# Kernel optimization log

Hardware: AMD Instinct MI355X
Metric: run time of the kernel (lower is better)

The kernel has to match this reference:

```python
import jax, jax.numpy as jnp
import numpy as np

B, S, WIDTH, M = 2, 240, 128, 20
PAD = 16


def setup_inputs() -> dict:
    key = jax.random.key(0)
    ks = jax.random.split(key, 10)
    scale = 1.0 / (WIDTH * WIDTH)
    inp = {
        "x": jax.random.normal(ks[0], (B, S, S, 3), jnp.float32),
        "fc0_w": jax.random.normal(ks[1], (5, WIDTH), jnp.float32) * 0.1,
        "fc0_b": jnp.zeros((WIDTH,), jnp.float32),
        # 5 spectral layers, complex weights stored as [..., 2] = (real, imag)
        "spec_w1": jax.random.uniform(ks[2], (5, WIDTH, WIDTH, M, M, 2), jnp.float32) * scale,
        "spec_w2": jax.random.uniform(ks[3], (5, WIDTH, WIDTH, M, M, 2), jnp.float32) * scale,
        # 5 residual 1x1 convs
        "w_w": jax.random.normal(ks[4], (5, WIDTH, WIDTH), jnp.float32) / np.sqrt(WIDTH),
        "w_b": jnp.zeros((5, WIDTH), jnp.float32),
        "fc1_w": jax.random.normal(ks[5], (WIDTH, WIDTH), jnp.float32) / np.sqrt(WIDTH),
        "fc1_b": jnp.zeros((WIDTH,), jnp.float32),
        # 4 heads (u, v, p, T): width->64->1
        "head1_w": jax.random.normal(ks[6], (4, WIDTH, 64), jnp.float32) / np.sqrt(WIDTH),
        "head1_b": jnp.zeros((4, 64), jnp.float32),
        "head2_w": jax.random.normal(ks[7], (4, 64, 1), jnp.float32) / 8.0,
        "head2_b": jnp.zeros((4, 1), jnp.float32),
    }
    return inp


def _spectral_conv(h, w1, w2):
    # h: (B, C, H, W) real; w1, w2: (C_in, C_out, M, M) complex64
    Hh, Ww = h.shape[-2], h.shape[-1]
    ft = jnp.fft.rfft2(h)  # (B, C, H, W//2+1)
    o1 = jnp.einsum('bixy,ioxy->boxy', ft[:, :, :M, :M], w1)
    o2 = jnp.einsum('bixy,ioxy->boxy', ft[:, :, -M:, :M], w2)
    out_ft = jnp.zeros((h.shape[0], w1.shape[1], Hh, Ww // 2 + 1), jnp.complex64)
    out_ft = out_ft.at[:, :, :M, :M].set(o1).at[:, :, -M:, :M].set(o2)
    return jnp.fft.irfft2(out_ft, s=(Hh, Ww))


def reference(x, fc0_w, fc0_b, spec_w1, spec_w2, w_w, w_b, fc1_w, fc1_b,
              head1_w, head1_b, head2_w, head2_b):
    Bn, sx, sy = x.shape[0], x.shape[1], x.shape[2]
    gx = jnp.broadcast_to(jnp.linspace(0.0, 1.0, sx, dtype=x.dtype)[None, :, None, None], (Bn, sx, sy, 1))
    gy = jnp.broadcast_to(jnp.linspace(0.0, 1.0, sy, dtype=x.dtype)[None, None, :, None], (Bn, sx, sy, 1))
    x1 = jnp.concatenate([x, gx, gy], axis=-1)          # (B, S, S, 5)
    h = x1 @ fc0_w + fc0_b                              # lift -> (B, S, S, width)
    h = jnp.transpose(h, (0, 3, 1, 2))                  # (B, width, S, S)
    h = jnp.pad(h, ((0, 0), (0, 0), (0, PAD), (0, PAD)))
    c1 = spec_w1[..., 0] + 1j * spec_w1[..., 1]
    c2 = spec_w2[..., 0] + 1j * spec_w2[..., 1]
    for i in range(5):
        s = _spectral_conv(h, c1[i], c2[i])
        lin = jnp.einsum('bchw,oc->bohw', h, w_w[i]) + w_b[i][None, :, None, None]
        h = s + lin
        if i < 4:
            h = jax.nn.gelu(h, approximate=False)
    h = h[..., :-PAD, :-PAD]
    h = jnp.transpose(h, (0, 2, 3, 1))                  # (B, S, S, width)
    h = jax.nn.gelu(h @ fc1_w + fc1_b, approximate=False)
    h1 = jax.nn.gelu(jnp.einsum('bhwc,kcd->kbhwd', h, head1_w)
                     + head1_b[:, None, None, None, :], approximate=False)
    out = jnp.einsum('kbhwd,kdo->kbhwo', h1, head2_w) + head2_b[:, None, None, None, :]
    return (out[0], out[1], out[2], out[3])  # u, v, p, T each (B, S, S, 1)
```

## Files before the change

kernel.cpp:

```cpp
#include <hip/hip_runtime.h>
#include <math.h>


#define SZ_H   (2ull*256*256*128)
#define O_HA   0ull
#define O_HB   (O_HA + SZ_H)
#define O_G    (O_HB + SZ_H)
#define SZ_G   (2ull*256*20*128*2)
#define O_FTT  (O_G + SZ_G)
#define SZ_FT  (2ull*40*20*128*2)
#define O_OFT  (O_FTT + SZ_FT)
#define O_EY   (O_OFT + SZ_FT)
#define SZ_EY  (256ull*20*2)
#define O_EX   (O_EY + SZ_EY)
#define SZ_EX  (256ull*40*2)
#define O_EXI  (O_EX + SZ_EX)
#define O_WWT  (O_EXI + SZ_EX)
#define SZ_WWT 81920ull
#define O_PART (O_WWT + SZ_WWT)
#define SZ_PART (8ull*204800*2)
#define FC1_B_NEED (O_G + 6356992ull)

static __device__ __forceinline__ float gelu_f(float v) {
    return 0.5f * v * (1.0f + erff(v * 0.70710678118654752f));
}

__global__ void k_prep(const float* __restrict__ w_w, float* __restrict__ ws) {
    int i = blockIdx.x * 256 + threadIdx.x;
    const float STEP = 6.2831853071795864769f / 256.0f;
    if (i < 5120) {
        int ky = i % 20, y = i / 20;
        int t = (ky * y) & 255;
        float th = t * STEP;
        ws[O_EY + 2*(size_t)i]     = cosf(th);
        ws[O_EY + 2*(size_t)i + 1] = -sinf(th);
    } else if (i < 15360) {
        int m = i - 5120; int j = m % 40, x = m / 40;
        int kx = (j < 20) ? j : (216 + j);
        int t = (kx * x) & 255;
        float th = t * STEP;
        ws[O_EX + 2*(size_t)m]     = cosf(th);
        ws[O_EX + 2*(size_t)m + 1] = -sinf(th);
    } else if (i < 25600) {
        int m = i - 15360; int j = m % 40, x = m / 40;
        int kx = (j < 20) ? j : (216 + j);
        int t = (kx * x) & 255;
        float th = t * STEP;
        ws[O_EXI + 2*(size_t)m]     = cosf(th);
        ws[O_EXI + 2*(size_t)m + 1] = sinf(th);
    } else {
        int m = i - 25600;
        if (m < 81920) {
            int l = m >> 14, r = m & 16383;
            int ic = r >> 7, oc = r & 127;
            ws[O_WWT + m] = w_w[(size_t)l*16384 + oc*128 + ic];
        }
    }
}

__global__ __launch_bounds__(256) void k_fc0(const float* __restrict__ xin,
        const float* __restrict__ w, const float* __restrict__ bv,
        float4* __restrict__ H4) {
    size_t e = (size_t)blockIdx.x * 256 + threadIdx.x;
    int c4 = (int)(e & 31) * 4;
    int y = (int)((e >> 5) & 255);
    int x = (int)((e >> 13) & 255);
    int b = (int)(e >> 21);
    float4 h = make_float4(0.f, 0.f, 0.f, 0.f);
    if (x < 240 && y < 240) {
        const float* xp = xin + (((size_t)(b*240 + x))*240 + y)*3;
        float x0 = xp[0], x1 = xp[1], x2 = xp[2];
        float gx = x*(1.0f/239.0f), gy = y*(1.0f/239.0f);
        float4 w0 = *(const float4*)&w[c4];
        float4 w1 = *(const float4*)&w[128 + c4];
        float4 w2 = *(const float4*)&w[256 + c4];
        float4 w3 = *(const float4*)&w[384 + c4];
        float4 w4 = *(const float4*)&w[512 + c4];
        float4 bb = *(const float4*)&bv[c4];
        h.x = bb.x + x0*w0.x + x1*w1.x + x2*w2.x + gx*w3.x + gy*w4.x;
        h.y = bb.y + x0*w0.y + x1*w1.y + x2*w2.y + gx*w3.y + gy*w4.y;
        h.z = bb.z + x0*w0.z + x1*w1.z + x2*w2.z + gx*w3.z + gy*w4.z;
        h.w = bb.w + x0*w0.w + x1*w1.w + x2*w2.w + gx*w3.w + gy*w4.w;
    }
    H4[e] = h;
}

__global__ __launch_bounds__(256) void k_ydft(const float* __restrict__ H,
        const float* __restrict__ Ey, float2* __restrict__ G) {
    int b = blockIdx.x >> 8, x = blockIdx.x & 255;
    int c = threadIdx.x & 127;
    int yq = __builtin_amdgcn_readfirstlane((int)(threadIdx.x >> 7));
    const float* Hrow = H + ((size_t)(b*256 + x)) * 256 * 128;
    float ar[20], ai[20];
    #pragma unroll
    for (int k = 0; k < 20; k++) { ar[k] = 0.f; ai[k] = 0.f; }
    for (int i = 0; i < 128; i++) {
        int y = yq*128 + i;
        float v = Hrow[(size_t)y*128 + c];
        const float* e = Ey + (size_t)y*40;
        #pragma unroll
        for (int k = 0; k < 20; k++) {
            ar[k] = fmaf(v, e[2*k],   ar[k]);
            ai[k] = fmaf(v, e[2*k+1], ai[k]);
        }
    }
    __shared__ float red[20][128][2];
    if (yq == 1) {
        #pragma unroll
        for (int k = 0; k < 20; k++) { red[k][c][0] = ar[k]; red[k][c][1] = ai[k]; }
    }
    __syncthreads();
    if (yq == 0) {
        float2* Gp = G + ((size_t)(b*256 + x))*20*128;
        #pragma unroll
        for (int k = 0; k < 20; k++)
            Gp[k*128 + c] = make_float2(ar[k] + red[k][c][0], ai[k] + red[k][c][1]);
    }
}

__global__ __launch_bounds__(512) void k_xdft(const float2* __restrict__ G,
        const float* __restrict__ Ex, float2* __restrict__ ftT) {
    int t = blockIdx.x;
    int ch = t & 1, jq = (t >> 1) & 1, ky = (t >> 2) % 20, b = t / 80;
    int cl = threadIdx.x & 63;
    int xq = __builtin_amdgcn_readfirstlane((int)(threadIdx.x >> 6));
    int c = ch*64 + cl;
    int j0 = jq * 20;
    float ar[20], ai[20];
    #pragma unroll
    for (int k = 0; k < 20; k++) { ar[k] = 0.f; ai[k] = 0.f; }
    for (int i = 0; i < 32; i++) {
        int x = xq*32 + i;
        float2 g = G[(((size_t)(b*256 + x))*20 + ky)*128 + c];
        const float* e = Ex + (size_t)x*80 + j0*2;
        #pragma unroll
        for (int k = 0; k < 20; k++) {
            float er = e[2*k], ei = e[2*k+1];
            ar[k] = fmaf(g.x, er, fmaf(-g.y, ei, ar[k]));
            ai[k] = fmaf(g.x, ei, fmaf( g.y, er, ai[k]));
        }
    }
    __shared__ float red[4][20][64][2];
    if (xq >= 4) {
        int s = xq - 4;
        #pragma unroll
        for (int k = 0; k < 20; k++) { red[s][k][cl][0] = ar[k]; red[s][k][cl][1] = ai[k]; }
    }
    __syncthreads();
    if (xq < 4) {
        #pragma unroll
        for (int k = 0; k < 20; k++) { ar[k] += red[xq][k][cl][0]; ai[k] += red[xq][k][cl][1]; }
    }
    __syncthreads();
    if (xq == 2 || xq == 3) {
        int s = xq - 2;
        #pragma unroll
        for (int k = 0; k < 20; k++) { red[s][k][cl][0] = ar[k]; red[s][k][cl][1] = ai[k]; }
    }
    __syncthreads();
    if (xq < 2) {
        #pragma unroll
        for (int k = 0; k < 20; k++) { ar[k] += red[xq][k][cl][0]; ai[k] += red[xq][k][cl][1]; }
    }
    __syncthreads();
    if (xq == 1) {
        #pragma unroll
        for (int k = 0; k < 20; k++) { red[0][k][cl][0] = ar[k]; red[0][k][cl][1] = ai[k]; }
    }
    __syncthreads();
    if (xq == 0) {
        #pragma unroll
        for (int k = 0; k < 20; k++) {
            float rr = ar[k] + red[0][k][cl][0];
            float ii = ai[k] + red[0][k][cl][1];
            ftT[((size_t)c*2 + b)*800 + (size_t)(j0 + k)*20 + ky] = make_float2(rr, ii);
        }
    }
}

__global__ __launch_bounds__(448) void k_modemix(const float2* __restrict__ w1,
        const float2* __restrict__ w2, const float2* __restrict__ ftT,
        float2* __restrict__ outp, int ic_per) {
    int bid = blockIdx.x & 255;
    int icq = blockIdx.x >> 8;
    int oc = bid >> 1;
    int mh = bid & 1;
    int tid = threadIdx.x;
    if (tid >= 400) return;
    int wsel = tid / 200;
    int m = mh*200 + (tid % 200);
    int jk = wsel*400 + m;
    const float2* wb = wsel ? w2 : w1;
    int ic0 = icq * ic_per;
    float ar0=0.f, ai0=0.f, ar1=0.f, ai1=0.f;
    #pragma unroll 4
    for (int i = 0; i < ic_per; i++) {
        int ic = ic0 + i;
        float2 wv = wb[((size_t)(ic*128 + oc))*400 + m];
        float2 f0 = ftT[(size_t)ic*1600 + jk];
        float2 f1 = ftT[(size_t)ic*1600 + 800 + jk];
        ar0 = fmaf(f0.x, wv.x, fmaf(-f0.y, wv.y, ar0));
        ai0 = fmaf(f0.x, wv.y, fmaf( f0.y, wv.x, ai0));
        ar1 = fmaf(f1.x, wv.x, fmaf(-f1.y, wv.y, ar1));
        ai1 = fmaf(f1.x, wv.y, fmaf( f1.y, wv.x, ai1));
    }
    float2* o = outp + (size_t)icq * 204800;
    o[(size_t)jk*128 + oc]         = make_float2(ar0, ai0);
    o[(size_t)(800 + jk)*128 + oc] = make_float2(ar1, ai1);
}

__global__ __launch_bounds__(512) void k_modered(const float2* __restrict__ part,
        float2* __restrict__ oft) {
    int i = blockIdx.x * 512 + threadIdx.x;
    if (i >= 204800) return;
    float2 s = part[i];
    #pragma unroll
    for (int q = 1; q < 8; q++) {
        float2 p = part[(size_t)q*204800 + i];
        s.x += p.x; s.y += p.y;
    }
    oft[i] = s;
}

__global__ __launch_bounds__(256) void k_xidft(const float2* __restrict__ oft,
        const float* __restrict__ Exi, float2* __restrict__ T) {
    int b = blockIdx.x >> 7, xq = blockIdx.x & 127;
    int oc = threadIdx.x & 127;
    int xs = __builtin_amdgcn_readfirstlane((int)(threadIdx.x >> 7));
    int x = xq*2 + xs;
    float ar[20], ai[20];
    #pragma unroll
    for (int k = 0; k < 20; k++) { ar[k] = 0.f; ai[k] = 0.f; }
    const float2* ob = oft + (size_t)b*800*128;
    for (int j = 0; j < 40; j++) {
        float er = Exi[(size_t)x*80 + 2*j], ei = Exi[(size_t)x*80 + 2*j + 1];
        #pragma unroll
        for (int k = 0; k < 20; k++) {
            float2 o = ob[(size_t)(j*20 + k)*128 + oc];
            ar[k] = fmaf(o.x, er, fmaf(-o.y, ei, ar[k]));
            ai[k] = fmaf(o.x, ei, fmaf( o.y, er, ai[k]));
        }
    }
    float2* Tp = T + ((size_t)(b*256 + x))*20*128;
    #pragma unroll
    for (int k = 0; k < 20; k++) Tp[k*128 + oc] = make_float2(ar[k], ai[k]);
}

__global__ __launch_bounds__(256) void k_spec_lin(const float* __restrict__ H,
        const float2* __restrict__ T, const float* __restrict__ wwT,
        const float* __restrict__ wb, float* __restrict__ Hout, int do_gelu) {
    int yg = blockIdx.x & 3;
    int x  = (blockIdx.x >> 2) & 255;
    int b  = blockIdx.x >> 10;
    int tid = threadIdx.x;
    int lane = tid & 63;
    int wv = __builtin_amdgcn_readfirstlane(tid >> 6);
    int oc0 = wv * 32;
    int y0 = yg * 64;
    __shared__ float hl[64][129];
    const float* Hbase = H + (((size_t)(b*256 + x))*256 + y0)*128;
    #pragma unroll
    for (int it = 0; it < 8; it++) {
        int i = tid + it*256;
        int pi = i >> 5, c4 = (i & 31)*4;
        float4 v = *(const float4*)&Hbase[(size_t)pi*128 + c4];
        hl[pi][c4] = v.x; hl[pi][c4+1] = v.y; hl[pi][c4+2] = v.z; hl[pi][c4+3] = v.w;
    }
    float csr[20], csi[20];
    {
        int y = y0 + lane;
        #pragma unroll
        for (int k = 0; k < 20; k++) {
            int t = (k * y) & 255;
            float th = t * (6.2831853071795864769f/256.0f);
            float f = (k == 0 ? 1.0f : 2.0f) * (1.0f/65536.0f);
            csr[k] = f * __cosf(th);
            csi[k] = f * __sinf(th);
        }
    }
    __syncthreads();
    float acc[32];
    #pragma unroll
    for (int o = 0; o < 32; o++) acc[o] = 0.f;
    for (int ic = 0; ic < 128; ic++) {
        float t = hl[lane][ic];
        const float* wr = &wwT[(size_t)ic*128 + oc0];
        #pragma unroll
        for (int o4 = 0; o4 < 8; o4++) {
            float4 w = *(const float4*)&wr[o4*4];
            acc[o4*4]   = fmaf(t, w.x, acc[o4*4]);
            acc[o4*4+1] = fmaf(t, w.y, acc[o4*4+1]);
            acc[o4*4+2] = fmaf(t, w.z, acc[o4*4+2]);
            acc[o4*4+3] = fmaf(t, w.w, acc[o4*4+3]);
        }
    }
    const float2* Tp = T + ((size_t)(b*256 + x))*20*128 + oc0;
    for (int k = 0; k < 20; k++) {
        const float2* tr = Tp + (size_t)k*128;
        float cr = csr[k], ci = csi[k];
        #pragma unroll
        for (int o = 0; o < 32; o++) {
            float2 tv = tr[o];
            acc[o] = fmaf(tv.x, cr, fmaf(-tv.y, ci, acc[o]));
        }
    }
    __syncthreads();
    const float* bp = &wb[oc0];
    #pragma unroll
    for (int o = 0; o < 32; o++) {
        float v = acc[o] + bp[o];
        if (do_gelu) v = gelu_f(v);
        hl[lane][oc0 + o] = v;
    }
    __syncthreads();
    float* Obase = Hout + (((size_t)(b*256 + x))*256 + y0)*128;
    #pragma unroll
    for (int it = 0; it < 32; it++) {
        int i = tid + it*256;
        int pi = i >> 7, c = i & 127;
        Obase[(size_t)pi*128 + c] = hl[pi][c];
    }
}

__global__ __launch_bounds__(128) void k_fc1(const float* __restrict__ H,
        const float* __restrict__ fc1_w, const float* __restrict__ fc1_b,
        float* __restrict__ outA, float* __restrict__ outB) {
    int tid = threadIdx.x;
    int lane = tid & 63;
    int wv = __builtin_amdgcn_readfirstlane(tid >> 6);
    int p0 = blockIdx.x * 64;
    __shared__ float hl[64][129];
    #pragma unroll
    for (int it = 0; it < 16; it++) {
        int i = tid + it*128;
        int pi = i >> 5, c4 = (i & 31)*4;
        int p = p0 + pi;
        int bb = p / 57600, r = p % 57600;
        int xx = r / 240, yy = r % 240;
        float4 v = *(const float4*)&H[(((size_t)(bb*256 + xx))*256 + yy)*128 + c4];
        hl[pi][c4] = v.x; hl[pi][c4+1] = v.y; hl[pi][c4+2] = v.z; hl[pi][c4+3] = v.w;
    }
    __syncthreads();
    int oc0 = wv*64;
    float acc[64];
    #pragma unroll
    for (int o = 0; o < 64; o++) acc[o] = 0.f;
    for (int ic = 0; ic < 128; ic++) {
        float t = hl[lane][ic];
        const float* wr = &fc1_w[(size_t)ic*128 + oc0];
        #pragma unroll
        for (int o4 = 0; o4 < 16; o4++) {
            float4 w = *(const float4*)&wr[o4*4];
            acc[o4*4]   = fmaf(t, w.x, acc[o4*4]);
            acc[o4*4+1] = fmaf(t, w.y, acc[o4*4+1]);
            acc[o4*4+2] = fmaf(t, w.z, acc[o4*4+2]);
            acc[o4*4+3] = fmaf(t, w.w, acc[o4*4+3]);
        }
    }
    __syncthreads();
    const float* bp = &fc1_b[oc0];
    #pragma unroll
    for (int o = 0; o < 64; o++) hl[lane][oc0 + o] = gelu_f(acc[o] + bp[o]);
    __syncthreads();
    float* outp = (p0 < 65536) ? (outA + (size_t)p0*128)
                               : (outB + ((size_t)(p0 - 65536))*128);
    #pragma unroll
    for (int it = 0; it < 64; it++) {
        int i = tid + it*128;
        int pi = i >> 7, c = i & 127;
        outp[(size_t)pi*128 + c] = hl[pi][c];
    }
}

__global__ __launch_bounds__(256) void k_heads(const float* __restrict__ inA,
        const float* __restrict__ inB, const float* __restrict__ h1w,
        const float* __restrict__ h1b, const float* __restrict__ h2w,
        const float* __restrict__ h2b, float* __restrict__ out) {
    int tid = threadIdx.x;
    int lane = tid & 63;
    int k = __builtin_amdgcn_readfirstlane(tid >> 6);
    int p0 = blockIdx.x * 64;
    __shared__ float tl[128][65];
    const float* inp = (p0 < 65536) ? (inA + (size_t)p0*128)
                                    : (inB + ((size_t)(p0 - 65536))*128);
    #pragma unroll
    for (int it = 0; it < 8; it++) {
        int i = tid + it*256;
        int pi = i >> 5, c4 = (i & 31)*4;
        float4 v = *(const float4*)&inp[(size_t)pi*128 + c4];
        tl[c4][pi] = v.x; tl[c4+1][pi] = v.y; tl[c4+2][pi] = v.z; tl[c4+3][pi] = v.w;
    }
    __syncthreads();
    float acc[64];
    #pragma unroll
    for (int d = 0; d < 64; d++) acc[d] = 0.f;
    const float* wk = h1w + (size_t)k*8192;
    for (int c = 0; c < 128; c++) {
        float t = tl[c][lane];
        const float* wr = &wk[c*64];
        #pragma unroll
        for (int d4 = 0; d4 < 16; d4++) {
            float4 w = *(const float4*)&wr[d4*4];
            acc[d4*4]   = fmaf(t, w.x, acc[d4*4]);
            acc[d4*4+1] = fmaf(t, w.y, acc[d4*4+1]);
            acc[d4*4+2] = fmaf(t, w.z, acc[d4*4+2]);
            acc[d4*4+3] = fmaf(t, w.w, acc[d4*4+3]);
        }
    }
    const float* b1 = &h1b[k*64];
    const float* w2 = &h2w[k*64];
    float res = 0.f;
    #pragma unroll
    for (int d = 0; d < 64; d++)
        res += gelu_f(acc[d] + b1[d]) * w2[d];
    out[(size_t)k*115200 + p0 + lane] = res + h2b[k];
}

__global__ __launch_bounds__(256) void k_head(const float* __restrict__ H,
        const float* __restrict__ fc1_w, const float* __restrict__ fc1_b,
        const float* __restrict__ h1w, const float* __restrict__ h1b,
        const float* __restrict__ h2w, const float* __restrict__ h2b,
        float* __restrict__ out) {
    int tid = threadIdx.x;
    int p0 = blockIdx.x * 64;
    __shared__ float hl[64][128];
    __shared__ float tl[128][65];
    #pragma unroll
    for (int it = 0; it < 8; it++) {
        int i = tid + it*256;
        int pi = i >> 5, c4 = (i & 31)*4;
        int p = p0 + pi;
        int b = p / 57600, r = p % 57600;
        int xx = r / 240, yy = r % 240;
        *(float4*)&hl[pi][c4] = *(const float4*)&H[(((size_t)(b*256 + xx))*256 + yy)*128 + c4];
    }
    __syncthreads();
    {
        int ocg = tid & 31, pxg = tid >> 5;
        int oc0 = ocg*4, px0 = pxg*8;
        float acc[4][8];
        #pragma unroll
        for (int q = 0; q < 4; q++)
            #pragma unroll
            for (int p = 0; p < 8; p++) acc[q][p] = 0.f;
        for (int icc = 0; icc < 32; icc++) {
            float4 hv[8];
            #pragma unroll
            for (int p = 0; p < 8; p++) hv[p] = *(float4*)&hl[px0 + p][icc*4];
            float4 wA = *(const float4*)&fc1_w[(size_t)(icc*4+0)*128 + oc0];
            float4 wB = *(const float4*)&fc1_w[(size_t)(icc*4+1)*128 + oc0];
            float4 wC = *(const float4*)&fc1_w[(size_t)(icc*4+2)*128 + oc0];
            float4 wD = *(const float4*)&fc1_w[(size_t)(icc*4+3)*128 + oc0];
            #pragma unroll
            for (int p = 0; p < 8; p++) {
                float4 h4 = hv[p];
                acc[0][p] = fmaf(h4.x, wA.x, fmaf(h4.y, wB.x, fmaf(h4.z, wC.x, fmaf(h4.w, wD.x, acc[0][p]))));
                acc[1][p] = fmaf(h4.x, wA.y, fmaf(h4.y, wB.y, fmaf(h4.z, wC.y, fmaf(h4.w, wD.y, acc[1][p]))));
                acc[2][p] = fmaf(h4.x, wA.z, fmaf(h4.y, wB.z, fmaf(h4.z, wC.z, fmaf(h4.w, wD.z, acc[2][p]))));
                acc[3][p] = fmaf(h4.x, wA.w, fmaf(h4.y, wB.w, fmaf(h4.z, wC.w, fmaf(h4.w, wD.w, acc[3][p]))));
            }
        }
        float4 bb = *(const float4*)&fc1_b[oc0];
        float bq[4] = {bb.x, bb.y, bb.z, bb.w};
        #pragma unroll
        for (int q = 0; q < 4; q++)
            #pragma unroll
            for (int p = 0; p < 8; p++)
                tl[oc0 + q][px0 + p] = gelu_f(acc[q][p] + bq[q]);
    }
    __syncthreads();
    {
        int k = tid >> 6, dg = tid & 15, pxg = (tid >> 4) & 3;
        int d0 = dg*4, px0 = pxg*16;
        float acc2[4][16];
        #pragma unroll
        for (int q = 0; q < 4; q++)
            #pragma unroll
            for (int i = 0; i < 16; i++) acc2[q][i] = 0.f;
        const float* wp = h1w + (size_t)k*8192 + d0;
        for (int c = 0; c < 128; c++) {
            float4 w = *(const float4*)&wp[(size_t)c*64];
            #pragma unroll
            for (int i = 0; i < 16; i++) {
                float v = tl[c][px0 + i];
                acc2[0][i] = fmaf(v, w.x, acc2[0][i]);
                acc2[1][i] = fmaf(v, w.y, acc2[1][i]);
                acc2[2][i] = fmaf(v, w.z, acc2[2][i]);
                acc2[3][i] = fmaf(v, w.w, acc2[3][i]);
            }
        }
        float4 b1 = *(const float4*)&h1b[k*64 + d0];
        float4 w2 = *(const float4*)&h2w[k*64 + d0];
        float ob = h2b[k];
        #pragma unroll
        for (int i = 0; i < 16; i++) {
            float u = gelu_f(acc2[0][i] + b1.x) * w2.x
                    + gelu_f(acc2[1][i] + b1.y) * w2.y
                    + gelu_f(acc2[2][i] + b1.z) * w2.z
                    + gelu_f(acc2[3][i] + b1.w) * w2.w;
            u += __shfl_down(u, 8);
            u += __shfl_down(u, 4);
            u += __shfl_down(u, 2);
            u += __shfl_down(u, 1);
            if (dg == 0) out[(size_t)k*115200 + p0 + px0 + i] = u + ob;
        }
    }
}

extern "C" void kernel_launch(void* const* d_in, const int* in_sizes, int n_in,
                              void* d_out, int out_size, void* d_ws, size_t ws_size,
                              hipStream_t stream) {
    const float* x       = (const float*)d_in[0];
    const float* fc0_w   = (const float*)d_in[1];
    const float* fc0_b   = (const float*)d_in[2];
    const float* spec_w1 = (const float*)d_in[3];
    const float* spec_w2 = (const float*)d_in[4];
    const float* w_w     = (const float*)d_in[5];
    const float* w_b     = (const float*)d_in[6];
    const float* fc1_w   = (const float*)d_in[7];
    const float* fc1_b   = (const float*)d_in[8];
    const float* head1_w = (const float*)d_in[9];
    const float* head1_b = (const float*)d_in[10];
    const float* head2_w = (const float*)d_in[11];
    const float* head2_b = (const float*)d_in[12];
    float* ws = (float*)d_ws;
    float* out = (float*)d_out;

    int split      = ws_size >= (size_t)(O_PART + SZ_PART) * 4 ? 1 : 0;
    int head_split = ws_size >= (size_t)FC1_B_NEED * 4 ? 1 : 0;

    k_prep<<<420, 256, 0, stream>>>(w_w, ws);
    k_fc0<<<16384, 256, 0, stream>>>(x, fc0_w, fc0_b, (float4*)(ws + O_HA));

    float* cur = ws + O_HA;
    float* nxt = ws + O_HB;
    float2* G    = (float2*)(ws + O_G);
    float2* ftT  = (float2*)(ws + O_FTT);
    float2* oft  = (float2*)(ws + O_OFT);
    float2* part = (float2*)(ws + O_PART);

    for (int l = 0; l < 5; l++) {
        k_ydft<<<512, 256, 0, stream>>>(cur, ws + O_EY, G);
        k_xdft<<<160, 512, 0, stream>>>(G, ws + O_EX, ftT);
        const float2* w1l = (const float2*)(spec_w1 + (size_t)l*13107200);
        const float2* w2l = (const float2*)(spec_w2 + (size_t)l*13107200);
        if (split) {
            k_modemix<<<2048, 448, 0, stream>>>(w1l, w2l, ftT, part, 16);
            k_modered<<<400, 512, 0, stream>>>(part, oft);
        } else {
            k_modemix<<<256, 448, 0, stream>>>(w1l, w2l, ftT, oft, 128);
        }
        k_xidft<<<256, 256, 0, stream>>>(oft, ws + O_EXI, G);
        k_spec_lin<<<2048, 256, 0, stream>>>(cur, G, ws + O_WWT + (size_t)l*16384,
                                             w_b + l*128, nxt, (l < 4) ? 1 : 0);
        float* t = cur; cur = nxt; nxt = t;
    }
    if (head_split) {
        float* fA = ws + O_HA;
        float* fB = ws + O_G;
        k_fc1<<<1800, 128, 0, stream>>>(cur, fc1_w, fc1_b, fA, fB);
        k_heads<<<1800, 256, 0, stream>>>(fA, fB, head1_w, head1_b,
                                          head2_w, head2_b, out);
    } else {
        k_head<<<1800, 256, 0, stream>>>(cur, fc1_w, fc1_b, head1_w, head1_b,
                                         head2_w, head2_b, out);
    }
}
```

Measured before the change: 1.960 ms.

## Fuse fc1 and heads into one tail kernel and repartition x-DFT blocks

Merges the separate fc1 and heads kernels into one 512-thread kernel. The fc1 output stays in shared memory (transposed) and feeds the four heads directly, so the intermediate activation no longer makes a global round trip. Also splits the x-direction DFT over four times as many smaller blocks, with fewer accumulators per thread and a shuffle plus single shared-memory reduction step instead of a multi-stage barrier tree. The fused kernel's many global weight loads per thread, and the higher per-block register and LDS use, may limit occupancy.

```diff
diff --git a/kernel.cpp b/kernel.cpp
--- a/kernel.cpp
+++ b/kernel.cpp
@@ -19,7 +19,6 @@
 #define SZ_WWT 81920ull
 #define O_PART (O_WWT + SZ_WWT)
 #define SZ_PART (8ull*204800*2)
-#define FC1_B_NEED (O_G + 6356992ull)
 
 static __device__ __forceinline__ float gelu_f(float v) {
     return 0.5f * v * (1.0f + erff(v * 0.70710678118654752f));
@@ -118,61 +117,47 @@
     }
 }
 
-__global__ __launch_bounds__(512) void k_xdft(const float2* __restrict__ G,
+__global__ __launch_bounds__(256) void k_xdft(const float2* __restrict__ G,
         const float* __restrict__ Ex, float2* __restrict__ ftT) {
     int t = blockIdx.x;
-    int ch = t & 1, jq = (t >> 1) & 1, ky = (t >> 2) % 20, b = t / 80;
-    int cl = threadIdx.x & 63;
-    int xq = __builtin_amdgcn_readfirstlane((int)(threadIdx.x >> 6));
-    int c = ch*64 + cl;
-    int j0 = jq * 20;
-    float ar[20], ai[20];
-    #pragma unroll
-    for (int k = 0; k < 20; k++) { ar[k] = 0.f; ai[k] = 0.f; }
+    int ch = t & 3, jq = (t >> 2) & 3, ky = (t >> 4) % 20, b = t / 320;
+    int cl = threadIdx.x & 31;
+    int xq = threadIdx.x >> 5;
+    int c = ch*32 + cl;
+    int j0 = jq*10;
+    float ar[10], ai[10];
+    #pragma unroll
+    for (int k = 0; k < 10; k++) { ar[k] = 0.f; ai[k] = 0.f; }
     for (int i = 0; i < 32; i++) {
         int x = xq*32 + i;
         float2 g = G[(((size_t)(b*256 + x))*20 + ky)*128 + c];
-        const float* e = Ex + (size_t)x*80 + j0*2;
-        #pragma unroll
-        for (int k = 0; k < 20; k++) {
-            float er = e[2*k], ei = e[2*k+1];
-            ar[k] = fmaf(g.x, er, fmaf(-g.y, ei, ar[k]));
-            ai[k] = fmaf(g.x, ei, fmaf( g.y, er, ai[k]));
-        }
-    }
-    __shared__ float red[4][20][64][2];
-    if (xq >= 4) {
-        int s = xq - 4;
-        #pragma unroll
-        for (int k = 0; k < 20; k++) { red[s][k][cl][0] = ar[k]; red[s][k][cl][1] = ai[k]; }
-    }
-    __syncthreads();
-    if (xq < 4) {
-        #pragma unroll
-        for (int k = 0; k < 20; k++) { ar[k] += red[xq][k][cl][0]; ai[k] += red[xq][k][cl][1]; }
-    }
-    __syncthreads();
-    if (xq == 2 || xq == 3) {
-        int s = xq - 2;
-        #pragma unroll
-        for (int k = 0; k < 20; k++) { red[s][k][cl][0] = ar[k]; red[s][k][cl][1] = ai[k]; }
-    }
-    __syncthreads();
-    if (xq < 2) {
-        #pragma unroll
-        for (int k = 0; k < 20; k++) { ar[k] += red[xq][k][cl][0]; ai[k] += red[xq][k][cl][1]; }
-    }
-    __syncthreads();
-    if (xq == 1) {
-        #pragma unroll
-        for (int k = 0; k < 20; k++) { red[0][k][cl][0] = ar[k]; red[0][k][cl][1] = ai[k]; }
-    }
-    __syncthreads();
-    if (xq == 0) {
-        #pragma unroll
-        for (int k = 0; k < 20; k++) {
-            float rr = ar[k] + red[0][k][cl][0];
-            float ii = ai[k] + red[0][k][cl][1];
+        const float2* e2 = (const float2*)(Ex + (size_t)x*80) + j0;
+        #pragma unroll
+        for (int k = 0; k < 10; k++) {
+            float2 e = e2[k];
+            ar[k] = fmaf(g.x, e.x, fmaf(-g.y, e.y, ar[k]));
+            ai[k] = fmaf(g.x, e.y, fmaf( g.y, e.x, ai[k]));
+        }
+    }
+    #pragma unroll
+    for (int k = 0; k < 10; k++) {
+        ar[k] += __shfl_xor(ar[k], 32);
+        ai[k] += __shfl_xor(ai[k], 32);
+    }
+    __shared__ float red[3][10][32][2];
+    int wid = threadIdx.x >> 6;
+    int sub = threadIdx.x & 63;
+    if (wid > 0 && sub < 32) {
+        #pragma unroll
+        for (int k = 0; k < 10; k++) { red[wid-1][k][cl][0] = ar[k]; red[wid-1][k][cl][1] = ai[k]; }
+    }
+    __syncthreads();
+    if (wid == 0 && sub < 32) {
+        #pragma unroll
+        for (int k = 0; k < 10; k++) {
+            float rr = ar[k], ii = ai[k];
+            #pragma unroll
+            for (int q = 0; q < 3; q++) { rr += red[q][k][cl][0]; ii += red[q][k][cl][1]; }
             ftT[((size_t)c*2 + b)*800 + (size_t)(j0 + k)*20 + ky] = make_float2(rr, ii);
         }
     }
@@ -322,17 +307,22 @@
     }
 }
 
-__global__ __launch_bounds__(128) void k_fc1(const float* __restrict__ H,
+__global__ __launch_bounds__(512) void k_tail(const float* __restrict__ H,
         const float* __restrict__ fc1_w, const float* __restrict__ fc1_b,
-        float* __restrict__ outA, float* __restrict__ outB) {
+        const float* __restrict__ h1w, const float* __restrict__ h1b,
+        const float* __restrict__ h2w, const float* __restrict__ h2b,
+        float* __restrict__ out) {
     int tid = threadIdx.x;
     int lane = tid & 63;
     int wv = __builtin_amdgcn_readfirstlane(tid >> 6);
     int p0 = blockIdx.x * 64;
-    __shared__ float hl[64][129];
-    #pragma unroll
-    for (int it = 0; it < 16; it++) {
-        int i = tid + it*128;
+    __shared__ float smem[8320];
+    __shared__ float red[4][64];
+    float (*hl)[129] = (float (*)[129])smem;
+    float (*tl)[65]  = (float (*)[65])smem;
+    #pragma unroll
+    for (int it = 0; it < 4; it++) {
+        int i = tid + it*512;
         int pi = i >> 5, c4 = (i & 31)*4;
         int p = p0 + pi;
         int bb = p / 57600, r = p % 57600;
@@ -341,15 +331,16 @@
         hl[pi][c4] = v.x; hl[pi][c4+1] = v.y; hl[pi][c4+2] = v.z; hl[pi][c4+3] = v.w;
     }
     __syncthreads();
-    int oc0 = wv*64;
-    float acc[64];
-    #pragma unroll
-    for (int o = 0; o < 64; o++) acc[o] = 0.f;
+    int oc0 = wv * 16;
+    float acc[16];
+    #pragma unroll
+    for (int o = 0; o < 16; o++) acc[o] = 0.f;
+    #pragma unroll 2
     for (int ic = 0; ic < 128; ic++) {
         float t = hl[lane][ic];
         const float* wr = &fc1_w[(size_t)ic*128 + oc0];
         #pragma unroll
-        for (int o4 = 0; o4 < 16; o4++) {
+        for (int o4 = 0; o4 < 4; o4++) {
             float4 w = *(const float4*)&wr[o4*4];
             acc[o4*4]   = fmaf(t, w.x, acc[o4*4]);
             acc[o4*4+1] = fmaf(t, w.y, acc[o4*4+1]);
@@ -360,151 +351,39 @@
     __syncthreads();
     const float* bp = &fc1_b[oc0];
     #pragma unroll
-    for (int o = 0; o < 64; o++) hl[lane][oc0 + o] = gelu_f(acc[o] + bp[o]);
-    __syncthreads();
-    float* outp = (p0 < 65536) ? (outA + (size_t)p0*128)
-                               : (outB + ((size_t)(p0 - 65536))*128);
-    #pragma unroll
-    for (int it = 0; it < 64; it++) {
-        int i = tid + it*128;
-        int pi = i >> 7, c = i & 127;
-        outp[(size_t)pi*128 + c] = hl[pi][c];
-    }
-}
-
-__global__ __launch_bounds__(256) void k_heads(const float* __restrict__ inA,
-        const float* __restrict__ inB, const float* __restrict__ h1w,
-        const float* __restrict__ h1b, const float* __restrict__ h2w,
-        const float* __restrict__ h2b, float* __restrict__ out) {
-    int tid = threadIdx.x;
-    int lane = tid & 63;
-    int k = __builtin_amdgcn_readfirstlane(tid >> 6);
-    int p0 = blockIdx.x * 64;
-    __shared__ float tl[128][65];
-    const float* inp = (p0 < 65536) ? (inA + (size_t)p0*128)
-                                    : (inB + ((size_t)(p0 - 65536))*128);
-    #pragma unroll
-    for (int it = 0; it < 8; it++) {
-        int i = tid + it*256;
-        int pi = i >> 5, c4 = (i & 31)*4;
-        float4 v = *(const float4*)&inp[(size_t)pi*128 + c4];
-        tl[c4][pi] = v.x; tl[c4+1][pi] = v.y; tl[c4+2][pi] = v.z; tl[c4+3][pi] = v.w;
-    }
-    __syncthreads();
-    float acc[64];
-    #pragma unroll
-    for (int d = 0; d < 64; d++) acc[d] = 0.f;
-    const float* wk = h1w + (size_t)k*8192;
+    for (int o = 0; o < 16; o++)
+        tl[oc0 + o][lane] = gelu_f(acc[o] + bp[o]);
+    __syncthreads();
+    int k    = wv >> 1;
+    int half = wv & 1;
+    int d0 = half * 32;
+    float a2[32];
+    #pragma unroll
+    for (int d = 0; d < 32; d++) a2[d] = 0.f;
+    const float* wk = h1w + (size_t)k*8192 + d0;
+    #pragma unroll 2
     for (int c = 0; c < 128; c++) {
         float t = tl[c][lane];
         const float* wr = &wk[c*64];
         #pragma unroll
-        for (int d4 = 0; d4 < 16; d4++) {
+        for (int d4 = 0; d4 < 8; d4++) {
             float4 w = *(const float4*)&wr[d4*4];
-            acc[d4*4]   = fmaf(t, w.x, acc[d4*4]);
-            acc[d4*4+1] = fmaf(t, w.y, acc[d4*4+1]);
-            acc[d4*4+2] = fmaf(t, w.z, acc[d4*4+2]);
-            acc[d4*4+3] = fmaf(t, w.w, acc[d4*4+3]);
-        }
-    }
-    const float* b1 = &h1b[k*64];
-    const float* w2 = &h2w[k*64];
-    float res = 0.f;
-    #pragma unroll
-    for (int d = 0; d < 64; d++)
-        res += gelu_f(acc[d] + b1[d]) * w2[d];
-    out[(size_t)k*115200 + p0 + lane] = res + h2b[k];
-}
-
-__global__ __launch_bounds__(256) void k_head(const float* __restrict__ H,
-        const float* __restrict__ fc1_w, const float* __restrict__ fc1_b,
-        const float* __restrict__ h1w, const float* __restrict__ h1b,
-        const float* __restrict__ h2w, const float* __restrict__ h2b,
-        float* __restrict__ out) {
-    int tid = threadIdx.x;
-    int p0 = blockIdx.x * 64;
-    __shared__ float hl[64][128];
-    __shared__ float tl[128][65];
-    #pragma unroll
-    for (int it = 0; it < 8; it++) {
-        int i = tid + it*256;
-        int pi = i >> 5, c4 = (i & 31)*4;
-        int p = p0 + pi;
-        int b = p / 57600, r = p % 57600;
-        int xx = r / 240, yy = r % 240;
-        *(float4*)&hl[pi][c4] = *(const float4*)&H[(((size_t)(b*256 + xx))*256 + yy)*128 + c4];
-    }
-    __syncthreads();
-    {
-        int ocg = tid & 31, pxg = tid >> 5;
-        int oc0 = ocg*4, px0 = pxg*8;
-        float acc[4][8];
-        #pragma unroll
-        for (int q = 0; q < 4; q++)
-            #pragma unroll
-            for (int p = 0; p < 8; p++) acc[q][p] = 0.f;
-        for (int icc = 0; icc < 32; icc++) {
-            float4 hv[8];
-            #pragma unroll
-            for (int p = 0; p < 8; p++) hv[p] = *(float4*)&hl[px0 + p][icc*4];
-            float4 wA = *(const float4*)&fc1_w[(size_t)(icc*4+0)*128 + oc0];
-            float4 wB = *(const float4*)&fc1_w[(size_t)(icc*4+1)*128 + oc0];
-            float4 wC = *(const float4*)&fc1_w[(size_t)(icc*4+2)*128 + oc0];
-            float4 wD = *(const float4*)&fc1_w[(size_t)(icc*4+3)*128 + oc0];
-            #pragma unroll
-            for (int p = 0; p < 8; p++) {
-                float4 h4 = hv[p];
-                acc[0][p] = fmaf(h4.x, wA.x, fmaf(h4.y, wB.x, fmaf(h4.z, wC.x, fmaf(h4.w, wD.x, acc[0][p]))));
-                acc[1][p] = fmaf(h4.x, wA.y, fmaf(h4.y, wB.y, fmaf(h4.z, wC.y, fmaf(h4.w, wD.y, acc[1][p]))));
-                acc[2][p] = fmaf(h4.x, wA.z, fmaf(h4.y, wB.z, fmaf(h4.z, wC.z, fmaf(h4.w, wD.z, acc[2][p]))));
-                acc[3][p] = fmaf(h4.x, wA.w, fmaf(h4.y, wB.w, fmaf(h4.z, wC.w, fmaf(h4.w, wD.w, acc[3][p]))));
-            }
-        }
-        float4 bb = *(const float4*)&fc1_b[oc0];
-        float bq[4] = {bb.x, bb.y, bb.z, bb.w};
-        #pragma unroll
-        for (int q = 0; q < 4; q++)
-            #pragma unroll
-            for (int p = 0; p < 8; p++)
-                tl[oc0 + q][px0 + p] = gelu_f(acc[q][p] + bq[q]);
-    }
-    __syncthreads();
-    {
-        int k = tid >> 6, dg = tid & 15, pxg = (tid >> 4) & 3;
-        int d0 = dg*4, px0 = pxg*16;
-        float acc2[4][16];
-        #pragma unroll
-        for (int q = 0; q < 4; q++)
-            #pragma unroll
-            for (int i = 0; i < 16; i++) acc2[q][i] = 0.f;
-        const float* wp = h1w + (size_t)k*8192 + d0;
-        for (int c = 0; c < 128; c++) {
-            float4 w = *(const float4*)&wp[(size_t)c*64];
-            #pragma unroll
-            for (int i = 0; i < 16; i++) {
-                float v = tl[c][px0 + i];
-                acc2[0][i] = fmaf(v, w.x, acc2[0][i]);
-                acc2[1][i] = fmaf(v, w.y, acc2[1][i]);
-                acc2[2][i] = fmaf(v, w.z, acc2[2][i]);
-                acc2[3][i] = fmaf(v, w.w, acc2[3][i]);
-            }
-        }
-        float4 b1 = *(const float4*)&h1b[k*64 + d0];
-        float4 w2 = *(const float4*)&h2w[k*64 + d0];
-        float ob = h2b[k];
-        #pragma unroll
-        for (int i = 0; i < 16; i++) {
-            float u = gelu_f(acc2[0][i] + b1.x) * w2.x
-                    + gelu_f(acc2[1][i] + b1.y) * w2.y
-                    + gelu_f(acc2[2][i] + b1.z) * w2.z
-                    + gelu_f(acc2[3][i] + b1.w) * w2.w;
-            u += __shfl_down(u, 8);
-            u += __shfl_down(u, 4);
-            u += __shfl_down(u, 2);
-            u += __shfl_down(u, 1);
-            if (dg == 0) out[(size_t)k*115200 + p0 + px0 + i] = u + ob;
-        }
-    }
+            a2[d4*4]   = fmaf(t, w.x, a2[d4*4]);
+            a2[d4*4+1] = fmaf(t, w.y, a2[d4*4+1]);
+            a2[d4*4+2] = fmaf(t, w.z, a2[d4*4+2]);
+            a2[d4*4+3] = fmaf(t, w.w, a2[d4*4+3]);
+        }
+    }
+    const float* b1 = &h1b[k*64 + d0];
+    const float* w2 = &h2w[k*64 + d0];
+    float ph = 0.f;
+    #pragma unroll
+    for (int d = 0; d < 32; d++)
+        ph += gelu_f(a2[d] + b1[d]) * w2[d];
+    if (half == 1) red[k][lane] = ph;
+    __syncthreads();
+    if (half == 0)
+        out[(size_t)k*115200 + p0 + lane] = ph + red[k][lane] + h2b[k];
 }
 
 extern "C" void kernel_launch(void* const* d_in, const int* in_sizes, int n_in,
@@ -526,8 +405,7 @@
     float* ws = (float*)d_ws;
     float* out = (float*)d_out;
 
-    int split      = ws_size >= (size_t)(O_PART + SZ_PART) * 4 ? 1 : 0;
-    int head_split = ws_size >= (size_t)FC1_B_NEED * 4 ? 1 : 0;
+    int split = ws_size >= (size_t)(O_PART + SZ_PART) * 4 ? 1 : 0;
 
     k_prep<<<420, 256, 0, stream>>>(w_w, ws);
     k_fc0<<<16384, 256, 0, stream>>>(x, fc0_w, fc0_b, (float4*)(ws + O_HA));
@@ -541,7 +419,7 @@
 
     for (int l = 0; l < 5; l++) {
         k_ydft<<<512, 256, 0, stream>>>(cur, ws + O_EY, G);
-        k_xdft<<<160, 512, 0, stream>>>(G, ws + O_EX, ftT);
+        k_xdft<<<640, 256, 0, stream>>>(G, ws + O_EX, ftT);
         const float2* w1l = (const float2*)(spec_w1 + (size_t)l*13107200);
         const float2* w2l = (const float2*)(spec_w2 + (size_t)l*13107200);
         if (split) {
@@ -555,14 +433,6 @@
                                              w_b + l*128, nxt, (l < 4) ? 1 : 0);
         float* t = cur; cur = nxt; nxt = t;
     }
-    if (head_split) {
-        float* fA = ws + O_HA;
-        float* fB = ws + O_G;
-        k_fc1<<<1800, 128, 0, stream>>>(cur, fc1_w, fc1_b, fA, fB);
-        k_heads<<<1800, 256, 0, stream>>>(fA, fB, head1_w, head1_b,
-                                          head2_w, head2_b, out);
-    } else {
-        k_head<<<1800, 256, 0, stream>>>(cur, fc1_w, fc1_b, head1_w, head1_b,
-                                         head2_w, head2_b, out);
-    }
-}
+    k_tail<<<1800, 512, 0, stream>>>(cur, fc1_w, fc1_b, head1_w, head1_b,
+                                     head2_w, head2_b, out);
+}
```

After: 1.875 ms. 1.05x faster.
